# Optimization experiments

Measured on AMD Instinct MI355X. Metric: run time of the kernel, lower is better.

The kernel has to match this reference:

```python
import jax, jax.numpy as jnp
import numpy as np
from jax import lax

FPS_NUM = 512
GROUP_NUM = 32
RADIUS = 0.2
BIG = 1e10


def setup_inputs() -> dict:
    key = jax.random.key(0)
    k1, k2 = jax.random.split(key)
    B, N = 8, 32768
    xyz = jax.random.normal(k1, (B, N, 3), dtype=jnp.float32)
    farthest_init = jax.random.randint(k2, (B,), 0, N, dtype=jnp.int32)
    return {"xyz": xyz, "farthest_init": farthest_init}


def _fps(xyz, farthest_init):
    # xyz: [B, N, 3] -> centroids [B, FPS_NUM] int32
    B, N, _ = xyz.shape
    batch_ix = jnp.arange(B)

    def step(carry, _):
        distance, farthest = carry          # [B,N], [B]
        centroid = xyz[batch_ix, farthest]  # [B,3]
        dist = jnp.sum((xyz - centroid[:, None, :]) ** 2, axis=-1)  # [B,N]
        distance = jnp.minimum(distance, dist)
        new_farthest = jnp.argmax(distance, axis=1).astype(farthest.dtype)
        return (distance, new_farthest), farthest

    init = (jnp.full((B, N), BIG, dtype=xyz.dtype), farthest_init)
    _, centroids_t = lax.scan(step, init, None, length=FPS_NUM)  # [FPS_NUM, B]
    return centroids_t.T  # [B, FPS_NUM]


def _ball_query(xyz, centroids_xyz):
    # xyz [B,N,3], centroids_xyz [B,S,3] -> idx [B,S,GROUP_NUM]
    # Pairwise squared distances: [B, S, N]
    dist = jnp.sum((xyz[:, None, :, :] - centroids_xyz[:, :, None, :]) ** 2, axis=-1)
    dist = jnp.where(dist > RADIUS ** 2, BIG, dist)
    idx = jnp.argsort(dist, axis=-1)[:, :, :GROUP_NUM]
    return idx


def reference(xyz, farthest_init):
    centroids = _fps(xyz, farthest_init)                              # [B, S]
    centroids_xyz = jnp.take_along_axis(xyz, centroids[:, :, None], axis=1)  # [B, S, 3]
    group_idx = _ball_query(xyz, centroids_xyz)                       # [B, S, G]
    # gather grouped points per batch: xyz[b][group_idx[b]] -> [B, S, G, 3]
    grouped_xyz = jax.vmap(lambda pts, ix: pts[ix])(xyz, group_idx)
    relative_xyz = grouped_xyz - centroids_xyz[:, :, None, :]
    combined_points = jnp.concatenate(
        [centroids_xyz[:, :, None, :], relative_xyz], axis=2)         # [B, S, G+1, 3]
    return combined_points, centroids_xyz
```

## Files before the change

### kernel.cpp

```cpp
#include <hip/hip_runtime.h>
#include <stdint.h>

#define NPTS   32768
#define NBATCH 8
#define NFPS   512
#define NGRP   32
#define BIGF   1e10f
#define R2F    0.04f
#define CAP    512
#define QPB    8

#define THR    1024

typedef unsigned long long u64;

#define AWR(dst, src) asm volatile("v_accvgpr_write_b32 %0, %1" : "=a"(dst) : "v"(src));
#define ARD(dst, src) asm volatile("v_accvgpr_read_b32 %0, %1" : "=v"(dst) : "a"(src));

__attribute__((amdgpu_flat_work_group_size(THR, THR), amdgpu_waves_per_eu(4, 4)))
__global__ void fps_kernel(
    const float* __restrict__ xyz,
    const int* __restrict__ finit,
    int* __restrict__ cidx)
{
#pragma clang fp contract(off)
    const int b = blockIdx.x;
    const int t = threadIdx.x;
    const float* __restrict__ base = xyz + (size_t)b * (NPTS * 3);

    __shared__ float4 zs4[NPTS / 4];
    __shared__ float redM[2][16];
    __shared__ int   winBox[2];

    float AX0,AX1,AX2,AX3,AX4,AX5,AX6,AX7,AX8,AX9,AX10,AX11,AX12,AX13,AX14,AX15,
          AX16,AX17,AX18,AX19,AX20,AX21,AX22,AX23,AX24,AX25,AX26,AX27,AX28,AX29,AX30,AX31;
    float AY0,AY1,AY2,AY3,AY4,AY5,AY6,AY7,AY8,AY9,AY10,AY11,AY12,AY13,AY14,AY15,
          AY16,AY17,AY18,AY19,AY20,AY21,AY22,AY23,AY24,AY25,AY26,AY27,AY28,AY29,AY30,AY31;
    float D0,D1,D2,D3,D4,D5,D6,D7,D8,D9,D10,D11,D12,D13,D14,D15,
          D16,D17,D18,D19,D20,D21,D22,D23,D24,D25,D26,D27,D28,D29,D30,D31;

    {
        const float4* __restrict__ g4 = reinterpret_cast<const float4*>(base);
#define INITJ(j, P0, P1, P2, P3) { \
        const int c = (j) * THR + t;              \
        const float4 q0 = g4[3 * c + 0]; \
        const float4 q1 = g4[3 * c + 1]; \
        const float4 q2 = g4[3 * c + 2]; \
        AWR(AX##P0, q0.x) AWR(AX##P1, q0.w) AWR(AX##P2, q1.z) AWR(AX##P3, q2.y) \
        AWR(AY##P0, q0.y) AWR(AY##P1, q1.x) AWR(AY##P2, q1.w) AWR(AY##P3, q2.z) \
        zs4[c] = make_float4(q0.z, q1.y, q2.x, q2.w); \
        D##P0 = BIGF; D##P1 = BIGF; D##P2 = BIGF; D##P3 = BIGF; \
    }
        INITJ(0, 0, 1, 2, 3)     INITJ(1, 4, 5, 6, 7)
        INITJ(2, 8, 9, 10, 11)   INITJ(3, 12, 13, 14, 15)
        INITJ(4, 16, 17, 18, 19) INITJ(5, 20, 21, 22, 23)
        INITJ(6, 24, 25, 26, 27) INITJ(7, 28, 29, 30, 31)
#undef INITJ
    }

    int far = finit[b];
    float cx = base[3 * far + 0];
    float cy = base[3 * far + 1];
    float cz = base[3 * far + 2];

    const int wid  = t >> 6;
    const int lane = t & 63;
    if (t == 0) { winBox[0] = 0x7fffffff; winBox[1] = 0x7fffffff; }
    __syncthreads();

    for (int it = 0; it < NFPS; ++it) {
        if (t == 0) cidx[b * NFPS + it] = far;
        if (it == NFPS - 1) break;
        const int p = it & 1;

        float vm0 = -1.0f, vm1 = -1.0f;

#define PT(zk, P, VM) { \
        float ax, ay; ARD(ax, AX##P) ARD(ay, AY##P) \
        const float dx = ax - cx; \
        const float dy = ay - cy; \
        const float dz = (zk) - cz; \
        float d = dx * dx + dy * dy; \
        d = d + dz * dz; \
        D##P = fminf(D##P, d); \
        VM = fmaxf(VM, D##P); \
    }
#define STEPJ(j, P0, P1, P2, P3) { \
        const float4 zq = zs4[(j) * THR + t];     \
        PT(zq.x, P0, vm0) PT(zq.y, P1, vm1) \
        PT(zq.z, P2, vm0) PT(zq.w, P3, vm1) \
    }
        STEPJ(0, 0, 1, 2, 3)     STEPJ(1, 4, 5, 6, 7)
        STEPJ(2, 8, 9, 10, 11)   STEPJ(3, 12, 13, 14, 15)
        STEPJ(4, 16, 17, 18, 19) STEPJ(5, 20, 21, 22, 23)
        STEPJ(6, 24, 25, 26, 27) STEPJ(7, 28, 29, 30, 31)
#undef STEPJ
#undef PT
        const float vmaxT = fmaxf(vm0, vm1);

        float wm = vmaxT;
#pragma unroll
        for (int off = 32; off >= 1; off >>= 1)
            wm = fmaxf(wm, __shfl_xor(wm, off, 64));
        if (lane == 0) redM[p][wid] = wm;
        __syncthreads();

        float bm = redM[p][lane & 15];
#pragma unroll
        for (int off = 8; off >= 1; off >>= 1)
            bm = fmaxf(bm, __shfl_xor(bm, off, 64));

        if (vmaxT == bm) {
            int best = 0x7fffffff;
#define RES(P) { \
            const int gi = (((P) >> 2) << 12) + (t << 2) + ((P) & 3); \
            if (D##P == bm) best = min(best, gi); \
        }
            RES(0)  RES(1)  RES(2)  RES(3)  RES(4)  RES(5)  RES(6)  RES(7)
            RES(8)  RES(9)  RES(10) RES(11) RES(12) RES(13) RES(14) RES(15)
            RES(16) RES(17) RES(18) RES(19) RES(20) RES(21) RES(22) RES(23)
            RES(24) RES(25) RES(26) RES(27) RES(28) RES(29) RES(30) RES(31)
#undef RES
            atomicMin(&winBox[p], best);
        }
        __syncthreads();

        far = winBox[p];
        if (t == 0) winBox[p ^ 1] = 0x7fffffff;
        far = __builtin_amdgcn_readfirstlane(far);
        cx = base[3 * far + 0];
        cy = base[3 * far + 1];
        cz = base[3 * far + 2];
    }
}

__global__ __launch_bounds__(256) void ballq_kernel(
    const float* __restrict__ xyz,
    const int* __restrict__ cidx,
    float* __restrict__ out0,
    float* __restrict__ out1)
{
#pragma clang fp contract(off)
    const int blk0 = blockIdx.x * QPB;
    const int b    = blk0 >> 9;
    const int t    = threadIdx.x;
    const float* __restrict__ base = xyz + (size_t)b * (NPTS * 3);

    __shared__ u64 list[QPB][CAP];
    __shared__ int scnt[QPB];
    __shared__ u64 mask0[QPB];
    __shared__ int selIdx[QPB][NGRP];

    if (t < QPB) scnt[t] = 0;

    float cxs[QPB], cys[QPB], czs[QPB];
#pragma unroll
    for (int q = 0; q < QPB; ++q) {
        const int ci = cidx[blk0 + q];
        cxs[q] = base[3 * ci + 0];
        cys[q] = base[3 * ci + 1];
        czs[q] = base[3 * ci + 2];
    }
    __syncthreads();

    if (t < 64) {
        const float px = base[3 * t + 0];
        const float py = base[3 * t + 1];
        const float pz = base[3 * t + 2];
#pragma unroll
        for (int q = 0; q < QPB; ++q) {
            float dx = px - cxs[q];
            float dy = py - cys[q];
            float dz = pz - czs[q];
            float d  = dx * dx + dy * dy;
            d = d + dz * dz;
            u64 mk = __ballot(d <= R2F);
            if (t == 0) mask0[q] = mk;
        }
    }

    for (int k = 0; k < NPTS / 256; ++k) {
        const int p = k * 256 + t;
        const float px = base[3 * p + 0];
        const float py = base[3 * p + 1];
        const float pz = base[3 * p + 2];
#pragma unroll
        for (int q = 0; q < QPB; ++q) {
            float dx = px - cxs[q];
            float dy = py - cys[q];
            float dz = pz - czs[q];
            float d  = dx * dx + dy * dy;
            d = d + dz * dz;
            if (d <= R2F) {
                int pos = atomicAdd(&scnt[q], 1);
                if (pos < CAP)
                    list[q][pos] = (((u64)__float_as_uint(d)) << 32)
                                   | (unsigned)p;
            }
        }
    }
    __syncthreads();

    {
        const int lane = t & 63;
        for (int q = t >> 6; q < QPB; q += 4) {
            const int m = min(scnt[q], CAP);
            for (int j = lane; j < m; j += 64) {
                const u64 kj = list[q][j];
                int rank = 0;
                for (int i = 0; i < m; ++i) rank += (list[q][i] < kj) ? 1 : 0;
                if (rank < NGRP) selIdx[q][rank] = (int)(kj & 0xffffffffu);
            }
        }
    }
    __syncthreads();

    for (int s = t; s < 33 * QPB; s += 256) {
        const int q    = s / 33;
        const int slot = s % 33;
        const int sg   = blk0 + q;
        const float cx = cxs[q], cy = cys[q], cz = czs[q];
        const size_t o0 = (size_t)sg * 33 * 3;
        if (slot == 32) {
            out0[o0 + 0] = cx; out0[o0 + 1] = cy; out0[o0 + 2] = cz;
            const size_t o1 = (size_t)sg * 3;
            out1[o1 + 0] = cx; out1[o1 + 1] = cy; out1[o1 + 2] = cz;
        } else {
            const int m = min(scnt[q], CAP);
            const int K = min(m, NGRP);
            int idx;
            if (slot < K) {
                idx = selIdx[q][slot];
            } else {
                u64 zeros = ~mask0[q];
                const int need = slot - K;
                for (int z = 0; z < need; ++z) zeros &= zeros - 1;
                idx = __builtin_ctzll(zeros);
            }
            const float px = base[3 * idx + 0];
            const float py = base[3 * idx + 1];
            const float pz = base[3 * idx + 2];
            out0[o0 + (size_t)(1 + slot) * 3 + 0] = px - cx;
            out0[o0 + (size_t)(1 + slot) * 3 + 1] = py - cy;
            out0[o0 + (size_t)(1 + slot) * 3 + 2] = pz - cz;
        }
    }
}

extern "C" void kernel_launch(void* const* d_in, const int* in_sizes, int n_in,
                              void* d_out, int out_size, void* d_ws, size_t ws_size,
                              hipStream_t stream) {
    const float* xyz   = (const float*)d_in[0];
    const int*   finit = (const int*)d_in[1];
    float* out0 = (float*)d_out;
    float* out1 = out0 + (size_t)NBATCH * NFPS * 33 * 3;

    int* cidx = (int*)d_ws;

    fps_kernel<<<NBATCH, THR, 0, stream>>>(xyz, finit, cidx);
    ballq_kernel<<<(NBATCH * NFPS) / QPB, 256, 0, stream>>>(xyz, cidx, out0, out1);
}
```

Baseline: 1.530 ms.

## Use LDS atomicMax for block max, prefetch z loads, and max3 reductions

Replaces the per-wave shared-memory max array and second shuffle reduction with an LDS atomicMax on the float bits, which is valid because distances are non-negative. It also software-prefetches the next z float4 from LDS, merges the running max into v_max3 instructions, and drops the waves_per_eu attribute. The goal is a shorter critical path per FPS iteration, which is latency-bound by reductions and barriers. In exchange it adds 16 contended LDS atomics per iteration and one more live register for the prefetch. It also gives up the explicit occupancy hint.

Result: faster. 1.438 ms (-6.0%).

```diff
diff --git a/kernel.cpp b/kernel.cpp
--- a/kernel.cpp
+++ b/kernel.cpp
@@ -16,8 +16,9 @@
 
 #define AWR(dst, src) asm volatile("v_accvgpr_write_b32 %0, %1" : "=a"(dst) : "v"(src));
 #define ARD(dst, src) asm volatile("v_accvgpr_read_b32 %0, %1" : "=v"(dst) : "a"(src));
-
-__attribute__((amdgpu_flat_work_group_size(THR, THR), amdgpu_waves_per_eu(4, 4)))
+#define MAX3(m, a, b) asm("v_max3_f32 %0, %0, %1, %2" : "+v"(m) : "v"(a), "v"(b));
+
+__attribute__((amdgpu_flat_work_group_size(THR, THR)))
 __global__ void fps_kernel(
     const float* __restrict__ xyz,
     const int* __restrict__ finit,
@@ -29,8 +30,8 @@
     const float* __restrict__ base = xyz + (size_t)b * (NPTS * 3);
 
     __shared__ float4 zs4[NPTS / 4];
-    __shared__ float redM[2][16];
-    __shared__ int   winBox[2];
+    __shared__ unsigned winMax[2];
+    __shared__ int      winIdx[2];
 
     float AX0,AX1,AX2,AX3,AX4,AX5,AX6,AX7,AX8,AX9,AX10,AX11,AX12,AX13,AX14,AX15,
           AX16,AX17,AX18,AX19,AX20,AX21,AX22,AX23,AX24,AX25,AX26,AX27,AX28,AX29,AX30,AX31;
@@ -63,9 +64,11 @@
     float cy = base[3 * far + 1];
     float cz = base[3 * far + 2];
 
-    const int wid  = t >> 6;
     const int lane = t & 63;
-    if (t == 0) { winBox[0] = 0x7fffffff; winBox[1] = 0x7fffffff; }
+    if (t == 0) {
+        winMax[0] = 0u; winMax[1] = 0u;
+        winIdx[0] = 0x7fffffff; winIdx[1] = 0x7fffffff;
+    }
     __syncthreads();
 
     for (int it = 0; it < NFPS; ++it) {
@@ -75,7 +78,7 @@
 
         float vm0 = -1.0f, vm1 = -1.0f;
 
-#define PT(zk, P, VM) { \
+#define PT(zk, P) { \
         float ax, ay; ARD(ax, AX##P) ARD(ay, AY##P) \
         const float dx = ax - cx; \
         const float dy = ay - cy; \
@@ -83,12 +86,14 @@
         float d = dx * dx + dy * dy; \
         d = d + dz * dz; \
         D##P = fminf(D##P, d); \
-        VM = fmaxf(VM, D##P); \
-    }
+    }
+        float4 zq = zs4[t];
 #define STEPJ(j, P0, P1, P2, P3) { \
-        const float4 zq = zs4[(j) * THR + t];     \
-        PT(zq.x, P0, vm0) PT(zq.y, P1, vm1) \
-        PT(zq.z, P2, vm0) PT(zq.w, P3, vm1) \
+        const float4 zc = zq; \
+        if ((j) < 7) zq = zs4[((j) + 1) * THR + t]; \
+        PT(zc.x, P0) PT(zc.y, P1) PT(zc.z, P2) PT(zc.w, P3) \
+        MAX3(vm0, D##P0, D##P1) \
+        MAX3(vm1, D##P2, D##P3) \
     }
         STEPJ(0, 0, 1, 2, 3)     STEPJ(1, 4, 5, 6, 7)
         STEPJ(2, 8, 9, 10, 11)   STEPJ(3, 12, 13, 14, 15)
@@ -102,13 +107,12 @@
 #pragma unroll
         for (int off = 32; off >= 1; off >>= 1)
             wm = fmaxf(wm, __shfl_xor(wm, off, 64));
-        if (lane == 0) redM[p][wid] = wm;
+        if (lane == 0) atomicMax(&winMax[p], __float_as_uint(wm));
         __syncthreads();
 
-        float bm = redM[p][lane & 15];
-#pragma unroll
-        for (int off = 8; off >= 1; off >>= 1)
-            bm = fmaxf(bm, __shfl_xor(bm, off, 64));
+        if (t == 0) { winMax[p ^ 1] = 0u; winIdx[p ^ 1] = 0x7fffffff; }
+
+        const float bm = __uint_as_float(winMax[p]);
 
         if (vmaxT == bm) {
             int best = 0x7fffffff;
@@ -121,13 +125,11 @@
             RES(16) RES(17) RES(18) RES(19) RES(20) RES(21) RES(22) RES(23)
             RES(24) RES(25) RES(26) RES(27) RES(28) RES(29) RES(30) RES(31)
 #undef RES
-            atomicMin(&winBox[p], best);
+            atomicMin(&winIdx[p], best);
         }
         __syncthreads();
 
-        far = winBox[p];
-        if (t == 0) winBox[p ^ 1] = 0x7fffffff;
-        far = __builtin_amdgcn_readfirstlane(far);
+        far = __builtin_amdgcn_readfirstlane(winIdx[p]);
         cx = base[3 * far + 0];
         cy = base[3 * far + 1];
         cz = base[3 * far + 2];
```
